# Kernel optimization log

Measured on AMD Instinct MI355X. Metric: run time of the kernel, lower is better.

## Reference

```python
import jax, jax.numpy as jnp
import numpy as np

# Each of the 16 binary logic gates, relaxed to real values, is a multilinear
# function: gate(a,b) = c0 + c1*a + c2*b + c3*a*b. Rows follow the standard
# difflogic ordering: FALSE, AND, a&~b, a, ~a&b, b, XOR, OR, NOR, XNOR,
# ~b, a|~b, ~a, ~a|b, NAND, TRUE.
GATE_COEF = jnp.array([
    [0.0,  0.0,  0.0,  0.0],   # 0:  false
    [0.0,  0.0,  0.0,  1.0],   # 1:  a AND b
    [0.0,  1.0,  0.0, -1.0],   # 2:  a AND NOT b
    [0.0,  1.0,  0.0,  0.0],   # 3:  a
    [0.0,  0.0,  1.0, -1.0],   # 4:  NOT a AND b
    [0.0,  0.0,  1.0,  0.0],   # 5:  b
    [0.0,  1.0,  1.0, -2.0],   # 6:  a XOR b
    [0.0,  1.0,  1.0, -1.0],   # 7:  a OR b
    [1.0, -1.0, -1.0,  1.0],   # 8:  NOR
    [1.0, -1.0, -1.0,  2.0],   # 9:  XNOR
    [1.0,  0.0, -1.0,  0.0],   # 10: NOT b
    [1.0,  0.0, -1.0,  1.0],   # 11: a OR NOT b
    [1.0, -1.0,  0.0,  0.0],   # 12: NOT a
    [1.0, -1.0,  0.0,  1.0],   # 13: NOT a OR b
    [1.0,  0.0,  0.0, -1.0],   # 14: NAND
    [1.0,  0.0,  0.0,  0.0],   # 15: true
], dtype=jnp.float32)

B, IN_DIM, HIDDEN, N_LAYERS, OUT_DIM, TAU = 4096, 1024, 8192, 6, 8, 10.0
NPO = HIDDEN // OUT_DIM  # neurons_per_output


def logic_layer(h, w, ia, ib):
    # h: [B, in_dim]; w: [H, 16]; ia, ib: [H] int indices into in_dim.
    # Softmax-weighted blend of 16 gates == multilinear form with blended coefs.
    p = jax.nn.softmax(w, axis=-1)          # [H, 16]
    c = p @ GATE_COEF                       # [H, 4]
    a = h[:, ia]                            # [B, H] gather
    b = h[:, ib]                            # [B, H] gather
    return c[:, 0] + c[:, 1] * a + c[:, 2] * b + c[:, 3] * (a * b)


def setup_inputs() -> dict:
    key = jax.random.key(0)
    ks = jax.random.split(key, 8)
    return {
        "x": jax.random.uniform(ks[0], (B, IN_DIM), dtype=jnp.float32),
        "logic_w": jax.random.normal(ks[1], (N_LAYERS, HIDDEN, 16), dtype=jnp.float32),
        "scaler_w": jax.random.normal(ks[2], (OUT_DIM, OUT_DIM), dtype=jnp.float32) * 0.1,
        "scaler_b": jax.random.normal(ks[3], (OUT_DIM,), dtype=jnp.float32) * 0.1,
        "idx0_a": jax.random.randint(ks[4], (HIDDEN,), 0, IN_DIM, dtype=jnp.int32),
        "idx0_b": jax.random.randint(ks[5], (HIDDEN,), 0, IN_DIM, dtype=jnp.int32),
        "idx_a": jax.random.randint(ks[6], (N_LAYERS - 1, HIDDEN), 0, HIDDEN, dtype=jnp.int32),
        "idx_b": jax.random.randint(ks[7], (N_LAYERS - 1, HIDDEN), 0, HIDDEN, dtype=jnp.int32),
    }


def reference(x, logic_w, scaler_w, scaler_b, idx0_a, idx0_b, idx_a, idx_b):
    h = (x.reshape(x.shape[0], -1) > 0.5).astype(jnp.float32)   # binarize
    h = logic_layer(h, logic_w[0], idx0_a, idx0_b)               # [B, HIDDEN]
    for i in range(N_LAYERS - 1):
        h = logic_layer(h, logic_w[i + 1], idx_a[i], idx_b[i])
    h = h.reshape(h.shape[0], OUT_DIM, NPO)                      # [B, O, NPO]
    values = jnp.sum(h, axis=2) / TAU                            # [B, O]
    q_values = values @ scaler_w.T + scaler_b                    # nn.Linear
    return q_values
```

## Files before the change

kernel.cpp:

```cpp
#include <hip/hip_runtime.h>
#include <hip/hip_fp16.h>

constexpr int BATCH    = 4096;
constexpr int IN_DIM   = 1024;
constexpr int HIDDEN   = 8192;
constexpr int N_LAYERS = 6;
constexpr int OUT_DIM  = 8;
constexpr float INV_TAU = 0.1f;

constexpr int TB   = 8;
constexpr int NTH  = 1024;
constexpr int NPT  = HIDDEN / NTH;
constexpr int NWAVES = NTH / 64;

__device__ __forceinline__ __half2 u2h(unsigned int u) {
    union { unsigned int u; __half2 h; } v; v.u = u; return v.h;
}
__device__ __forceinline__ unsigned int h2u(__half2 h) {
    union { unsigned int u; __half2 h; } v; v.h = h; return v.u;
}

__device__ __forceinline__ uint2 pack4(float4 v) {
    __half2 lo = __float22half2_rn(make_float2(v.x, v.y));
    __half2 hi = __float22half2_rn(make_float2(v.z, v.w));
    uint2 r; r.x = h2u(lo); r.y = h2u(hi); return r;
}

__global__ void prep_kernel(const float* __restrict__ logic_w,
                            const int* __restrict__ idx0_a,
                            const int* __restrict__ idx0_b,
                            const int* __restrict__ idx_a,
                            const int* __restrict__ idx_b,
                            uint2* __restrict__ coefp,
                            unsigned int* __restrict__ idxp, int n)
{
    int id = blockIdx.x * blockDim.x + threadIdx.x;
    if (id >= n) return;
    const int l = id / HIDDEN;
    const int j = id - l * HIDDEN;

    int ia, ib;
    if (l == 0) { ia = idx0_a[j]; ib = idx0_b[j]; }
    else        { ia = idx_a[(size_t)(l - 1) * HIDDEN + j];
                  ib = idx_b[(size_t)(l - 1) * HIDDEN + j]; }
    idxp[id] = (unsigned int)ia | ((unsigned int)ib << 16);

    const float4* w4 = (const float4*)(logic_w + (size_t)id * 16);
    float4 wa = w4[0], wb = w4[1], wc = w4[2], wd = w4[3];
    float wv[16] = {wa.x, wa.y, wa.z, wa.w, wb.x, wb.y, wb.z, wb.w,
                    wc.x, wc.y, wc.z, wc.w, wd.x, wd.y, wd.z, wd.w};
    float m = wv[0];
#pragma unroll
    for (int i = 1; i < 16; ++i) m = fmaxf(m, wv[i]);
    float e[16];
    float s = 0.f;
#pragma unroll
    for (int i = 0; i < 16; ++i) { e[i] = expf(wv[i] - m); s += e[i]; }
    float inv = 1.f / s;
    const float G0[16] = {0,0,0,0,0,0,0,0, 1,1,1,1,1,1,1,1};
    const float G1[16] = {0,0,1,1,0,0,1,1, -1,-1,0,0,-1,-1,0,0};
    const float G2[16] = {0,0,0,0,1,1,1,1, -1,-1,-1,-1,0,0,0,0};
    const float G3[16] = {0,1,-1,0,-1,0,-2,-1, 1,2,0,1,0,1,-1,0};
    float c0 = 0.f, c1 = 0.f, c2 = 0.f, c3 = 0.f;
#pragma unroll
    for (int i = 0; i < 16; ++i) {
        float p = e[i] * inv;
        c0 = fmaf(p, G0[i], c0);
        c1 = fmaf(p, G1[i], c1);
        c2 = fmaf(p, G2[i], c2);
        c3 = fmaf(p, G3[i], c3);
    }
    coefp[id] = pack4(make_float4(c0, c1, c2, c3));
}

__device__ __forceinline__ uint4 gate8(uint4 a, uint4 b, uint2 c) {
    __half2 cp01 = u2h(c.x), cp23 = u2h(c.y);
    __half2 c0 = __low2half2(cp01), c1 = __high2half2(cp01);
    __half2 c2 = __low2half2(cp23), c3 = __high2half2(cp23);
    uint4 r;
    {
        __half2 av = u2h(a.x), bv = u2h(b.x);
        r.x = h2u(__hfma2(bv, __hfma2(c3, av, c2), __hfma2(c1, av, c0)));
    }
    {
        __half2 av = u2h(a.y), bv = u2h(b.y);
        r.y = h2u(__hfma2(bv, __hfma2(c3, av, c2), __hfma2(c1, av, c0)));
    }
    {
        __half2 av = u2h(a.z), bv = u2h(b.z);
        r.z = h2u(__hfma2(bv, __hfma2(c3, av, c2), __hfma2(c1, av, c0)));
    }
    {
        __half2 av = u2h(a.w), bv = u2h(b.w);
        r.w = h2u(__hfma2(bv, __hfma2(c3, av, c2), __hfma2(c1, av, c0)));
    }
    return r;
}

__global__ __launch_bounds__(NTH) void net_kernel(
    const float*  __restrict__ x,
    const uint2*  __restrict__ coefp,
    const unsigned int* __restrict__ idxp,
    const float*  __restrict__ scaler_w, const float* __restrict__ scaler_b,
    float* __restrict__ out)
{
    __shared__ uint4 h[HIDDEN];
    __shared__ uint4 hx[IN_DIM];
    __shared__ float warr[NWAVES][TB];
    __shared__ float vals[TB][OUT_DIM];

    const int tid = threadIdx.x;
    const int b0  = blockIdx.x * TB;

    {
        float v[TB];
#pragma unroll
        for (int r = 0; r < TB; ++r)
            v[r] = (x[(size_t)(b0 + r) * IN_DIM + tid] > 0.5f) ? 1.f : 0.f;
        uint4 p;
        p.x = h2u(__floats2half2_rn(v[0], v[1]));
        p.y = h2u(__floats2half2_rn(v[2], v[3]));
        p.z = h2u(__floats2half2_rn(v[4], v[5]));
        p.w = h2u(__floats2half2_rn(v[6], v[7]));
        hx[tid] = p;
    }

    uint4 acc[NPT];
    unsigned int ij[NPT], ijn[NPT];
    uint2 cf[NPT], cfn[NPT];

#pragma unroll
    for (int k = 0; k < NPT; ++k) { ij[k] = idxp[k * NTH + tid]; cf[k] = coefp[k * NTH + tid]; }

    __syncthreads();

#pragma unroll
    for (int k = 0; k < NPT; ++k) {
        ijn[k] = idxp[HIDDEN + k * NTH + tid];
        cfn[k] = coefp[HIDDEN + k * NTH + tid];
    }
#pragma unroll
    for (int k = 0; k < NPT; ++k) {
        unsigned int pr = ij[k];
        acc[k] = gate8(hx[pr & 0xffffu], hx[pr >> 16], cf[k]);
    }
#pragma unroll
    for (int k = 0; k < NPT; ++k) h[k * NTH + tid] = acc[k];
    __syncthreads();

    for (int l = 1; l < N_LAYERS; ++l) {
#pragma unroll
        for (int k = 0; k < NPT; ++k) { ij[k] = ijn[k]; cf[k] = cfn[k]; }
        if (l < N_LAYERS - 1) {
#pragma unroll
            for (int k = 0; k < NPT; ++k) {
                ijn[k] = idxp[(size_t)(l + 1) * HIDDEN + k * NTH + tid];
                cfn[k] = coefp[(size_t)(l + 1) * HIDDEN + k * NTH + tid];
            }
        }
#pragma unroll
        for (int k = 0; k < NPT; ++k) {
            unsigned int pr = ij[k];
            acc[k] = gate8(h[pr & 0xffffu], h[pr >> 16], cf[k]);
        }
        __syncthreads();
#pragma unroll
        for (int k = 0; k < NPT; ++k) h[k * NTH + tid] = acc[k];
        __syncthreads();
    }

    {
        const int k    = tid >> 7;
        const int base = k * 1024 + (tid & 127);
        float s[TB] = {0.f, 0.f, 0.f, 0.f, 0.f, 0.f, 0.f, 0.f};
#pragma unroll
        for (int i = 0; i < 8; ++i) {
            uint4 t = h[base + 128 * i];
            float2 f0 = __half22float2(u2h(t.x));
            float2 f1 = __half22float2(u2h(t.y));
            float2 f2 = __half22float2(u2h(t.z));
            float2 f3 = __half22float2(u2h(t.w));
            s[0] += f0.x; s[1] += f0.y; s[2] += f1.x; s[3] += f1.y;
            s[4] += f2.x; s[5] += f2.y; s[6] += f3.x; s[7] += f3.y;
        }
#pragma unroll
        for (int off = 32; off > 0; off >>= 1) {
#pragma unroll
            for (int r = 0; r < TB; ++r) s[r] += __shfl_down(s[r], off);
        }
        if ((tid & 63) == 0) {
#pragma unroll
            for (int r = 0; r < TB; ++r) warr[tid >> 6][r] = s[r];
        }
    }
    __syncthreads();
    if (tid < TB * OUT_DIM) {
        int r = tid >> 3;
        int k = tid & 7;
        vals[r][k] = (warr[2 * k][r] + warr[2 * k + 1][r]) * INV_TAU;
    }
    __syncthreads();
    if (tid < TB * OUT_DIM) {
        int r = tid >> 3;
        int o = tid & 7;
        float q = scaler_b[o];
#pragma unroll
        for (int k = 0; k < OUT_DIM; ++k)
            q = fmaf(vals[r][k], scaler_w[o * OUT_DIM + k], q);
        out[(size_t)(b0 + r) * OUT_DIM + o] = q;
    }
}

extern "C" void kernel_launch(void* const* d_in, const int* in_sizes, int n_in,
                              void* d_out, int out_size, void* d_ws, size_t ws_size,
                              hipStream_t stream)
{
    const float* x        = (const float*)d_in[0];
    const float* logic_w  = (const float*)d_in[1];
    const float* scaler_w = (const float*)d_in[2];
    const float* scaler_b = (const float*)d_in[3];
    const int*   idx0_a   = (const int*)d_in[4];
    const int*   idx0_b   = (const int*)d_in[5];
    const int*   idx_a    = (const int*)d_in[6];
    const int*   idx_b    = (const int*)d_in[7];
    float* out = (float*)d_out;

    const int n = N_LAYERS * HIDDEN;
    uint2*        coefp = (uint2*)d_ws;
    unsigned int* idxp  = (unsigned int*)((char*)d_ws + (size_t)n * sizeof(uint2));

    prep_kernel<<<(n + 255) / 256, 256, 0, stream>>>(logic_w, idx0_a, idx0_b,
                                                     idx_a, idx_b, coefp, idxp, n);
    net_kernel<<<BATCH / TB, NTH, 0, stream>>>(x, coefp, idxp,
                                               scaler_w, scaler_b, out);
}
```

Before: 117.5 us.

## Store activations as fp8 with 16 batch rows per block and fuse last layer into reduction

Activations are packed as 16 fp8 values per uint4 instead of 8 fp16 values, so each block now handles 16 batch rows in the same shared memory and the grid halves. The gate math runs in fp32 after converting from fp8 with the hardware pack/unpack builtins. The last layer's outputs are accumulated straight into the per-output sums instead of being written to shared memory and read back. Neuron-to-thread mapping changes so each 128-thread group owns one output bucket, and coefficients are loaded just in time rather than prefetched. Storing the intermediate activations in fp8 loses precision and may exceed the accuracy tolerance.

```diff
diff --git a/kernel.cpp b/kernel.cpp
--- a/kernel.cpp
+++ b/kernel.cpp
@@ -8,18 +8,19 @@
 constexpr int OUT_DIM  = 8;
 constexpr float INV_TAU = 0.1f;
 
-constexpr int TB   = 8;
+constexpr int TB   = 16;
 constexpr int NTH  = 1024;
 constexpr int NPT  = HIDDEN / NTH;
 constexpr int NWAVES = NTH / 64;
 
+typedef float v2f __attribute__((ext_vector_type(2)));
+
 __device__ __forceinline__ __half2 u2h(unsigned int u) {
     union { unsigned int u; __half2 h; } v; v.u = u; return v.h;
 }
 __device__ __forceinline__ unsigned int h2u(__half2 h) {
     union { unsigned int u; __half2 h; } v; v.h = h; return v.u;
 }
-
 __device__ __forceinline__ uint2 pack4(float4 v) {
     __half2 lo = __float22half2_rn(make_float2(v.x, v.y));
     __half2 hi = __float22half2_rn(make_float2(v.z, v.w));
@@ -73,28 +74,37 @@
     coefp[id] = pack4(make_float4(c0, c1, c2, c3));
 }
 
-__device__ __forceinline__ uint4 gate8(uint4 a, uint4 b, uint2 c) {
+__device__ __forceinline__ void cvt16(uint4 p, float* f) {
+    const unsigned int* pd = (const unsigned int*)&p;
+#pragma unroll
+    for (int d = 0; d < 4; ++d) {
+        v2f lo = __builtin_amdgcn_cvt_pk_f32_fp8((int)pd[d], false);
+        v2f hi = __builtin_amdgcn_cvt_pk_f32_fp8((int)pd[d], true);
+        f[4 * d + 0] = lo.x; f[4 * d + 1] = lo.y;
+        f[4 * d + 2] = hi.x; f[4 * d + 3] = hi.y;
+    }
+}
+__device__ __forceinline__ uint4 pack16(const float* f) {
+    uint4 r;
+    unsigned int* rd = (unsigned int*)&r;
+#pragma unroll
+    for (int d = 0; d < 4; ++d) {
+        int w = __builtin_amdgcn_cvt_pk_fp8_f32(f[4 * d + 0], f[4 * d + 1], 0, false);
+        w     = __builtin_amdgcn_cvt_pk_fp8_f32(f[4 * d + 2], f[4 * d + 3], w, true);
+        rd[d] = (unsigned int)w;
+    }
+    return r;
+}
+
+__device__ __forceinline__ void gate16(uint4 a, uint4 b, uint2 c, float* r) {
     __half2 cp01 = u2h(c.x), cp23 = u2h(c.y);
-    __half2 c0 = __low2half2(cp01), c1 = __high2half2(cp01);
-    __half2 c2 = __low2half2(cp23), c3 = __high2half2(cp23);
-    uint4 r;
-    {
-        __half2 av = u2h(a.x), bv = u2h(b.x);
-        r.x = h2u(__hfma2(bv, __hfma2(c3, av, c2), __hfma2(c1, av, c0)));
-    }
-    {
-        __half2 av = u2h(a.y), bv = u2h(b.y);
-        r.y = h2u(__hfma2(bv, __hfma2(c3, av, c2), __hfma2(c1, av, c0)));
-    }
-    {
-        __half2 av = u2h(a.z), bv = u2h(b.z);
-        r.z = h2u(__hfma2(bv, __hfma2(c3, av, c2), __hfma2(c1, av, c0)));
-    }
-    {
-        __half2 av = u2h(a.w), bv = u2h(b.w);
-        r.w = h2u(__hfma2(bv, __hfma2(c3, av, c2), __hfma2(c1, av, c0)));
-    }
-    return r;
+    float c0 = __low2float(cp01),  c1 = __high2float(cp01);
+    float c2 = __low2float(cp23),  c3 = __high2float(cp23);
+    float fa[16], fb[16];
+    cvt16(a, fa); cvt16(b, fb);
+#pragma unroll
+    for (int i = 0; i < 16; ++i)
+        r[i] = fmaf(fb[i], fmaf(c3, fa[i], c2), fmaf(c1, fa[i], c0));
 }
 
 __global__ __launch_bounds__(NTH) void net_kernel(
@@ -111,87 +121,83 @@
 
     const int tid = threadIdx.x;
     const int b0  = blockIdx.x * TB;
+    const int g   = tid >> 7;
+    const int t0  = tid & 127;
+    const int jb  = g * 1024 + t0;
 
     {
         float v[TB];
 #pragma unroll
         for (int r = 0; r < TB; ++r)
             v[r] = (x[(size_t)(b0 + r) * IN_DIM + tid] > 0.5f) ? 1.f : 0.f;
-        uint4 p;
-        p.x = h2u(__floats2half2_rn(v[0], v[1]));
-        p.y = h2u(__floats2half2_rn(v[2], v[3]));
-        p.z = h2u(__floats2half2_rn(v[4], v[5]));
-        p.w = h2u(__floats2half2_rn(v[6], v[7]));
-        hx[tid] = p;
-    }
-
+        hx[tid] = pack16(v);
+    }
+
+    unsigned int ij[NPT], ijn[NPT];
     uint4 acc[NPT];
-    unsigned int ij[NPT], ijn[NPT];
-    uint2 cf[NPT], cfn[NPT];
-
-#pragma unroll
-    for (int k = 0; k < NPT; ++k) { ij[k] = idxp[k * NTH + tid]; cf[k] = coefp[k * NTH + tid]; }
-
-    __syncthreads();
-
-#pragma unroll
-    for (int k = 0; k < NPT; ++k) {
-        ijn[k] = idxp[HIDDEN + k * NTH + tid];
-        cfn[k] = coefp[HIDDEN + k * NTH + tid];
-    }
+
+#pragma unroll
+    for (int k = 0; k < NPT; ++k) ij[k] = idxp[jb + (k << 7)];
+
+    __syncthreads();
+
+#pragma unroll
+    for (int k = 0; k < NPT; ++k) ijn[k] = idxp[HIDDEN + jb + (k << 7)];
 #pragma unroll
     for (int k = 0; k < NPT; ++k) {
         unsigned int pr = ij[k];
-        acc[k] = gate8(hx[pr & 0xffffu], hx[pr >> 16], cf[k]);
-    }
-#pragma unroll
-    for (int k = 0; k < NPT; ++k) h[k * NTH + tid] = acc[k];
-    __syncthreads();
-
-    for (int l = 1; l < N_LAYERS; ++l) {
-#pragma unroll
-        for (int k = 0; k < NPT; ++k) { ij[k] = ijn[k]; cf[k] = cfn[k]; }
-        if (l < N_LAYERS - 1) {
-#pragma unroll
-            for (int k = 0; k < NPT; ++k) {
-                ijn[k] = idxp[(size_t)(l + 1) * HIDDEN + k * NTH + tid];
-                cfn[k] = coefp[(size_t)(l + 1) * HIDDEN + k * NTH + tid];
-            }
-        }
+        float rg[16];
+        gate16(hx[pr & 0xffffu], hx[pr >> 16], coefp[jb + (k << 7)], rg);
+        acc[k] = pack16(rg);
+    }
+#pragma unroll
+    for (int k = 0; k < NPT; ++k) h[jb + (k << 7)] = acc[k];
+    __syncthreads();
+
+    for (int l = 1; l < N_LAYERS - 1; ++l) {
+#pragma unroll
+        for (int k = 0; k < NPT; ++k) ij[k] = ijn[k];
+#pragma unroll
+        for (int k = 0; k < NPT; ++k)
+            ijn[k] = idxp[(size_t)(l + 1) * HIDDEN + jb + (k << 7)];
+        const uint2* cp = coefp + (size_t)l * HIDDEN;
 #pragma unroll
         for (int k = 0; k < NPT; ++k) {
             unsigned int pr = ij[k];
-            acc[k] = gate8(h[pr & 0xffffu], h[pr >> 16], cf[k]);
+            float rg[16];
+            gate16(h[pr & 0xffffu], h[pr >> 16], cp[jb + (k << 7)], rg);
+            acc[k] = pack16(rg);
         }
         __syncthreads();
 #pragma unroll
-        for (int k = 0; k < NPT; ++k) h[k * NTH + tid] = acc[k];
+        for (int k = 0; k < NPT; ++k) h[jb + (k << 7)] = acc[k];
         __syncthreads();
     }
 
+    float s[TB];
+#pragma unroll
+    for (int r = 0; r < TB; ++r) s[r] = 0.f;
     {
-        const int k    = tid >> 7;
-        const int base = k * 1024 + (tid & 127);
-        float s[TB] = {0.f, 0.f, 0.f, 0.f, 0.f, 0.f, 0.f, 0.f};
-#pragma unroll
-        for (int i = 0; i < 8; ++i) {
-            uint4 t = h[base + 128 * i];
-            float2 f0 = __half22float2(u2h(t.x));
-            float2 f1 = __half22float2(u2h(t.y));
-            float2 f2 = __half22float2(u2h(t.z));
-            float2 f3 = __half22float2(u2h(t.w));
-            s[0] += f0.x; s[1] += f0.y; s[2] += f1.x; s[3] += f1.y;
-            s[4] += f2.x; s[5] += f2.y; s[6] += f3.x; s[7] += f3.y;
+        const uint2* cp = coefp + (size_t)(N_LAYERS - 1) * HIDDEN;
+#pragma unroll
+        for (int k = 0; k < NPT; ++k) {
+            unsigned int pr = ijn[k];
+            float rg[16];
+            gate16(h[pr & 0xffffu], h[pr >> 16], cp[jb + (k << 7)], rg);
+#pragma unroll
+            for (int r = 0; r < TB; ++r) s[r] += rg[r];
         }
-#pragma unroll
-        for (int off = 32; off > 0; off >>= 1) {
-#pragma unroll
-            for (int r = 0; r < TB; ++r) s[r] += __shfl_down(s[r], off);
-        }
-        if ((tid & 63) == 0) {
-#pragma unroll
-            for (int r = 0; r < TB; ++r) warr[tid >> 6][r] = s[r];
-        }
+    }
+
+#pragma unroll
+    for (int off = 32; off > 0; off >>= 1) {
+#pragma unroll
+        for (int r = 0; r < TB; ++r) s[r] += __shfl_down(s[r], off);
+    }
+    if ((tid & 63) == 0) {
+        const int wv = tid >> 6;
+#pragma unroll
+        for (int r = 0; r < TB; ++r) warr[wv][r] = s[r];
     }
     __syncthreads();
     if (tid < TB * OUT_DIM) {
```

New measurement: 134.3 us. 14.3% more time.
